# Kernel optimization log

Hardware: AMD Instinct MI355X
Metric: run time of the kernel (lower is better)

The kernel has to match this reference:

```python
import jax, jax.numpy as jnp
import numpy as np

T, B, NA = 32, 32, 5          # timesteps, envs, actions
HID, FEAT = 256, 512          # lstm hidden, cnn features
IN_DIM = FEAT + NA            # lstm input size (517)
FLAT = 64 * 7 * 7             # cnn flatten size (3136)


def _conv(x, w, b, s):
    # x: NCHW, w: OIHW, VALID padding, stride s
    y = jax.lax.conv_general_dilated(x, w, (s, s), 'VALID',
                                     dimension_numbers=('NCHW', 'OIHW', 'NCHW'))
    return y + b[None, :, None, None]


def setup_inputs() -> dict:
    key = jax.random.key(0)
    ks = jax.random.split(key, 24)
    p = lambda k, shape: (jax.random.normal(k, shape, jnp.float32) * 0.05)
    return {
        'image': jax.random.uniform(ks[0], (T * B, 3, 84, 84), jnp.float32) * 255.0,
        'last_action': jax.random.randint(ks[1], (T * B,), 0, NA),
        'done': jax.random.bernoulli(ks[2], 0.05, (T * B,)).astype(jnp.float32),
        'h0': jnp.zeros((B, HID), jnp.float32),
        'c0': jnp.zeros((B, HID), jnp.float32),
        # NatureCNN params
        'W1': p(ks[3], (32, 3, 8, 8)), 'b1': jnp.zeros((32,), jnp.float32),
        'W2': p(ks[4], (64, 32, 4, 4)), 'b2': jnp.zeros((64,), jnp.float32),
        'W3': p(ks[5], (64, 64, 3, 3)), 'b3': jnp.zeros((64,), jnp.float32),
        'Wfc': p(ks[6], (FEAT, FLAT)), 'bfc': jnp.zeros((FEAT,), jnp.float32),
        # LSTM params (torch gate order i,f,g,o)
        'W_ih': p(ks[7], (4 * HID, IN_DIM)), 'W_hh': p(ks[8], (4 * HID, HID)),
        'b_ih': jnp.zeros((4 * HID,), jnp.float32), 'b_hh': jnp.zeros((4 * HID,), jnp.float32),
        # policy MLP (hidden 64, tanh)
        'Wp1': p(ks[9], (64, HID)), 'bp1': jnp.zeros((64,), jnp.float32),
        'Wp2': p(ks[10], (NA, 64)) * 0.01, 'bp2': jnp.zeros((NA,), jnp.float32),
        # value MLP
        'Wv1': p(ks[11], (64, HID)), 'bv1': jnp.zeros((64,), jnp.float32),
        'Wv2': p(ks[12], (1, 64)), 'bv2': jnp.zeros((1,), jnp.float32),
    }


def reference(image, last_action, done, h0, c0,
              W1, b1, W2, b2, W3, b3, Wfc, bfc,
              W_ih, W_hh, b_ih, b_hh,
              Wp1, bp1, Wp2, bp2, Wv1, bv1, Wv2, bv2):
    # --- extract: NatureCNN + one-hot(last_action) ---
    x = image / 255.0
    x = jax.nn.relu(_conv(x, W1, b1, 4))   # (TB,32,20,20)
    x = jax.nn.relu(_conv(x, W2, b2, 2))   # (TB,64,9,9)
    x = jax.nn.relu(_conv(x, W3, b3, 1))   # (TB,64,7,7)
    x = x.reshape(x.shape[0], -1)
    feat = jax.nn.relu(x @ Wfc.T + bfc)    # (TB,512)
    oh = jax.nn.one_hot(last_action, NA, dtype=feat.dtype)
    xs = jnp.concatenate([feat, oh], axis=1).reshape(T, B, IN_DIM)
    ds = done.reshape(T, B)

    # --- remember: done-masked LSTM recurrence (torch gate order i,f,g,o) ---
    def step(carry, inp):
        h, c = carry
        xt, dt = inp
        m = (1.0 - dt)[:, None]
        h = h * m
        c = c * m
        g = xt @ W_ih.T + b_ih + h @ W_hh.T + b_hh   # (B, 4*HID)
        i, f, gg, o = jnp.split(g, 4, axis=1)
        c = jax.nn.sigmoid(f) * c + jax.nn.sigmoid(i) * jnp.tanh(gg)
        h = jax.nn.sigmoid(o) * jnp.tanh(c)
        return (h, c), h

    (hT, cT), hs = jax.lax.scan(step, (h0, c0), (xs, ds))
    h = hs.reshape(T * B, HID)

    # --- heads ---
    logits = jnp.tanh(h @ Wp1.T + bp1) @ Wp2.T + bp2   # (TB, NA)
    v = jnp.tanh(h @ Wv1.T + bv1) @ Wv2.T + bv2        # (TB, 1)
    return logits, v, hT, cT
```

## Files before the change

### kernel.cpp

```cpp
#include <hip/hip_runtime.h>
#include <math.h>

typedef float  f4v __attribute__((ext_vector_type(4)));
typedef short  s8v __attribute__((ext_vector_type(8)));
typedef int    i4v __attribute__((ext_vector_type(4)));

__device__ __forceinline__ float sigm(float x) { return 1.f / (1.f + expf(-x)); }
__device__ __forceinline__ unsigned short f2bf(float f) {
    unsigned int u = __float_as_uint(f);
    return (unsigned short)((u + 0x7FFF + ((u >> 16) & 1)) >> 16);
}
__device__ __forceinline__ unsigned int cvt2(float lo, float hi) {
    unsigned int r;
    asm("v_cvt_pk_bf16_f32 %0, %1, %2" : "=v"(r) : "v"(lo), "v"(hi));
    return r;
}

__global__ __launch_bounds__(256) void k_amax(const float* __restrict__ Whh,
                                              unsigned int* __restrict__ amax_bits) {
    int i = blockIdx.x * 256 + threadIdx.x;
    float v = fabsf(Whh[i]);
#pragma unroll
    for (int o = 1; o < 64; o <<= 1) v = fmaxf(v, __shfl_xor(v, o));
    if ((threadIdx.x & 63) == 0) atomicMax(amax_bits, __float_as_uint(v));
}

__global__ __launch_bounds__(256) void k_prep(const float* __restrict__ W2, const float* __restrict__ W3,
                                              const float* __restrict__ Wfc, const float* __restrict__ Wih,
                                              const float* __restrict__ W1, const float* __restrict__ Whh,
                                              const unsigned int* __restrict__ amax_bits,
                                              unsigned short* __restrict__ W2p, unsigned short* __restrict__ W3p,
                                              unsigned short* __restrict__ Wfcp, unsigned short* __restrict__ Wihp,
                                              unsigned short* __restrict__ W1p, signed char* __restrict__ Wq) {
    int i = blockIdx.x * 256 + threadIdx.x;
    if (i < 32768) {
        int co = i >> 9, k = i & 511, t = k >> 5, ci = k & 31, ky = t >> 2, kx = t & 3;
        W2p[i] = f2bf(W2[co * 512 + ci * 16 + ky * 4 + kx]);
    } else if (i < 69632) {
        int j = i - 32768;
        int co = j / 576, k = j - co * 576, t = k >> 6, ci = k & 63;
        int ky = t / 3, kx = t - ky * 3;
        W3p[j] = f2bf(W3[((co * 64 + ci) * 3 + ky) * 3 + kx]);
    } else if (i < 1675264) {
        int j = i - 69632;
        Wfcp[j] = f2bf(Wfc[j]);
    } else if (i < 2199552) {
        int j = i - 1675264;
        int n = j >> 9, k = j & 511;
        Wihp[j] = f2bf(Wih[n * 517 + k]);
    } else if (i < 2205696) {
        int j = i - 2199552;
        W1p[j] = f2bf(W1[j] * (1.f / 255.f));
    } else if (i < 2467840) {
        int j = i - 2205696;
        float amax = __uint_as_float(amax_bits[0]);
        float s = 127.f / amax;
        int qv = (int)rintf(Whh[j] * s);
        qv = qv > 127 ? 127 : (qv < -127 ? -127 : qv);
        Wq[j] = (signed char)qv;
    }
}

__global__ __launch_bounds__(512) void k_conv1(const float* __restrict__ img,
                                               const unsigned short* __restrict__ Bw,
                                               const float* __restrict__ bias,
                                               unsigned short* __restrict__ out) {
    __shared__ unsigned short sImg[21168];
    int tid = threadIdx.x;
    int lane = tid & 63, w = tid >> 6;
    int l15 = lane & 15, q = lane >> 4;
    int im = blockIdx.x;
    const float4* srcv = (const float4*)(img + im * 21168);
    unsigned int* sW = (unsigned int*)sImg;
    for (int wi = tid; wi < 5292; wi += 512) {
        float4 v = srcv[wi];
        sW[wi * 2]     = cvt2(v.x, v.y);
        sW[wi * 2 + 1] = cvt2(v.z, v.w);
    }
    __syncthreads();
    const unsigned short* Bp0 = Bw + l15 * 192 + q * 8;
    const unsigned short* Bp1 = Bw + (16 + l15) * 192 + q * 8;
    s8v bf0[6], bf1[6];
#pragma unroll
    for (int ks = 0; ks < 6; ++ks) {
        bf0[ks] = *(const s8v*)(Bp0 + ks * 32);
        bf1[ks] = *(const s8v*)(Bp1 + ks * 32);
    }
    int woff[6];
#pragma unroll
    for (int ks = 0; ks < 6; ++ks) {
        int k0 = ks * 32 + q * 8;
        int c = k0 >> 6, ky = (k0 >> 3) & 7;
        woff[ks] = c * 7056 + ky * 84;
    }
    f4v acc[4][2];
#pragma unroll
    for (int i = 0; i < 4; ++i) { acc[i][0] = (f4v){0.f,0.f,0.f,0.f}; acc[i][1] = (f4v){0.f,0.f,0.f,0.f}; }
#pragma unroll
    for (int tt = 0; tt < 4; ++tt) {
        int t = w + tt * 8;
        if (t < 25) {
            int pA = t * 16 + l15;
            int oy = pA / 20, ox = pA - oy * 20;
            const unsigned short* ab = sImg + oy * 336 + ox * 4;
#pragma unroll
            for (int ks = 0; ks < 6; ++ks) {
                s8v a = *(const s8v*)(ab + woff[ks]);
                acc[tt][0] = __builtin_amdgcn_mfma_f32_16x16x32_bf16(a, bf0[ks], acc[tt][0], 0, 0, 0);
                acc[tt][1] = __builtin_amdgcn_mfma_f32_16x16x32_bf16(a, bf1[ks], acc[tt][1], 0, 0, 0);
            }
        }
    }
    __syncthreads();
    float b0v = bias[l15], b1v = bias[16 + l15];
#pragma unroll
    for (int tt = 0; tt < 4; ++tt) {
        int t = w + tt * 8;
        if (t < 25) {
            int pc = t * 16 + q * 4;
#pragma unroll
            for (int r = 0; r < 4; r += 2) {
                float v0 = acc[tt][0][r] + b0v;     v0 = v0 > 0.f ? v0 : 0.f;
                float v1 = acc[tt][0][r + 1] + b0v; v1 = v1 > 0.f ? v1 : 0.f;
                *(unsigned int*)&sImg[l15 * 404 + pc + r] = cvt2(v0, v1);
                float u0 = acc[tt][1][r] + b1v;     u0 = u0 > 0.f ? u0 : 0.f;
                float u1 = acc[tt][1][r + 1] + b1v; u1 = u1 > 0.f ? u1 : 0.f;
                *(unsigned int*)&sImg[(16 + l15) * 404 + pc + r] = cvt2(u0, u1);
            }
        }
    }
    __syncthreads();
    const unsigned int* cw = (const unsigned int*)sImg;
    unsigned int* ow = (unsigned int*)(out + im * 12800);
    for (int i = tid; i < 6400; i += 512) {
        int n = i / 200, rem = i - n * 200;
        ow[i] = cw[n * 202 + rem];
    }
}

__global__ __launch_bounds__(256, 2) void k_conv2(const unsigned short* __restrict__ A,
                                                  const unsigned short* __restrict__ Bw,
                                                  const float* __restrict__ bias,
                                                  unsigned short* __restrict__ out) {
    __shared__ unsigned short sA[800 * 32];
    __shared__ unsigned short c2s[64][196];
    int tid = threadIdx.x;
    int lane = tid & 63, w = tid >> 6;
    int l15 = lane & 15, q = lane >> 4;
    int img0 = blockIdx.x * 2;
    char* sAb = (char*)sA;
    const s8v* srcv = (const s8v*)(A + img0 * 12800);
    for (int wi = tid; wi < 3200; wi += 256) {
        s8v v = srcv[wi];
        int f = wi * 8;
        int im = f / 12800, r = f - im * 12800, ci = r / 400, p = r - ci * 400;
#pragma unroll
        for (int j = 0; j < 8; ++j) {
            int R = im * 400 + p + j;
            int Rl = (R >> 1) + (R & 1) * 400;
            int by = (Rl * 32 + ci) * 2 ^ ((Rl & 7) << 4);
            *(unsigned short*)(sAb + by) = (unsigned short)v[j];
        }
    }
    __syncthreads();
    int Rb[3];
#pragma unroll
    for (int mf = 0; mf < 3; ++mf) {
        int t = w * 3 + mf;
        int im = t / 6;
        int pp = (t - im * 6) * 16 + l15;
        int px = pp > 80 ? 80 : pp;
        int oy = px / 9, ox = px - oy * 9;
        Rb[mf] = im * 400 + oy * 40 + ox * 2;
    }
    const unsigned short* Bp0 = Bw + l15 * 512 + q * 8;
    const unsigned short* Bp1 = Bw + (16 + l15) * 512 + q * 8;
    const unsigned short* Bp2 = Bw + (32 + l15) * 512 + q * 8;
    const unsigned short* Bp3 = Bw + (48 + l15) * 512 + q * 8;
    f4v acc[3][4];
#pragma unroll
    for (int i = 0; i < 3; ++i)
#pragma unroll
        for (int j = 0; j < 4; ++j) acc[i][j] = (f4v){0.f, 0.f, 0.f, 0.f};
#pragma unroll
    for (int s = 0; s < 16; ++s) {
        const int ky = s >> 2, kx = s & 3;
        const int d = ky * 20 + kx;
        s8v a[3];
#pragma unroll
        for (int mf = 0; mf < 3; ++mf) {
            int R = Rb[mf] + d;
            int Rl = (R >> 1) + (R & 1) * 400;
            int by = (Rl * 64 + q * 16) ^ ((Rl & 7) << 4);
            a[mf] = *(const s8v*)(sAb + by);
        }
        s8v b0 = *(const s8v*)(Bp0 + s * 32);
        s8v b1 = *(const s8v*)(Bp1 + s * 32);
        s8v b2 = *(const s8v*)(Bp2 + s * 32);
        s8v b3 = *(const s8v*)(Bp3 + s * 32);
#pragma unroll
        for (int mf = 0; mf < 3; ++mf) {
            acc[mf][0] = __builtin_amdgcn_mfma_f32_16x16x32_bf16(a[mf], b0, acc[mf][0], 0, 0, 0);
            acc[mf][1] = __builtin_amdgcn_mfma_f32_16x16x32_bf16(a[mf], b1, acc[mf][1], 0, 0, 0);
            acc[mf][2] = __builtin_amdgcn_mfma_f32_16x16x32_bf16(a[mf], b2, acc[mf][2], 0, 0, 0);
            acc[mf][3] = __builtin_amdgcn_mfma_f32_16x16x32_bf16(a[mf], b3, acc[mf][3], 0, 0, 0);
        }
    }
#pragma unroll
    for (int nf = 0; nf < 4; ++nf) {
        int co = nf * 16 + l15;
        float b = bias[co];
#pragma unroll
        for (int mf = 0; mf < 3; ++mf) {
            int rr = (w * 3 + mf) * 16 + q * 4;
#pragma unroll
            for (int r = 0; r < 4; r += 2) {
                float v0 = acc[mf][nf][r] + b;     v0 = v0 > 0.f ? v0 : 0.f;
                float v1 = acc[mf][nf][r + 1] + b; v1 = v1 > 0.f ? v1 : 0.f;
                *(unsigned int*)&c2s[co][rr + r] = cvt2(v0, v1);
            }
        }
    }
    __syncthreads();
    for (int idx = tid; idx < 10368; idx += 256) {
        int im = idx / 5184, r2 = idx - im * 5184, co = r2 / 81, p = r2 - co * 81;
        out[(img0 + im) * 5184 + r2] = c2s[co][im * 96 + p];
    }
}

__global__ __launch_bounds__(256, 2) void k_conv3(const unsigned short* __restrict__ A,
                                                  const unsigned short* __restrict__ Bw,
                                                  const float* __restrict__ bias,
                                                  unsigned short* __restrict__ out) {
    __shared__ unsigned short sA[162 * 64];
    __shared__ unsigned short c3s[64][132];
    int tid = threadIdx.x;
    int lane = tid & 63, w = tid >> 6;
    int l15 = lane & 15, q = lane >> 4;
    int img0 = blockIdx.x * 2;
    char* sAb = (char*)sA;
    const s8v* srcv = (const s8v*)(A + img0 * 5184);
    for (int wi = tid; wi < 1296; wi += 256) {
        s8v v = srcv[wi];
        int f = wi * 8;
#pragma unroll
        for (int j = 0; j < 8; ++j) {
            int fe = f + j;
            int im = fe / 5184, r = fe - im * 5184, ci = r / 81, p = r - ci * 81;
            int R = im * 81 + p;
            int by = (R * 64 + ci) * 2 ^ ((R & 7) << 4);
            *(unsigned short*)(sAb + by) = (unsigned short)v[j];
        }
    }
    __syncthreads();
    int Rb[2];
#pragma unroll
    for (int mf = 0; mf < 2; ++mf) {
        int t = w * 2 + mf;
        int im = t >> 2;
        int pp = (t & 3) * 16 + l15;
        int px = pp > 48 ? 48 : pp;
        int oy = px / 7, ox = px - oy * 7;
        Rb[mf] = im * 81 + oy * 9 + ox;
    }
    const unsigned short* Bp0 = Bw + l15 * 576 + q * 8;
    const unsigned short* Bp1 = Bw + (16 + l15) * 576 + q * 8;
    const unsigned short* Bp2 = Bw + (32 + l15) * 576 + q * 8;
    const unsigned short* Bp3 = Bw + (48 + l15) * 576 + q * 8;
    f4v acc[2][4];
#pragma unroll
    for (int i = 0; i < 2; ++i)
#pragma unroll
        for (int j = 0; j < 4; ++j) acc[i][j] = (f4v){0.f, 0.f, 0.f, 0.f};
#pragma unroll
    for (int s = 0; s < 18; ++s) {
        const int tap = s >> 1, cb2 = (s & 1) * 64;
        const int ky = tap / 3, kx = tap - ky * 3;
        const int d = ky * 9 + kx;
        s8v a0, a1;
        {
            int R = Rb[0] + d;
            int by = (R * 128 + cb2 + q * 16) ^ ((R & 7) << 4);
            a0 = *(const s8v*)(sAb + by);
        }
        {
            int R = Rb[1] + d;
            int by = (R * 128 + cb2 + q * 16) ^ ((R & 7) << 4);
            a1 = *(const s8v*)(sAb + by);
        }
        s8v b0 = *(const s8v*)(Bp0 + s * 32);
        s8v b1 = *(const s8v*)(Bp1 + s * 32);
        s8v b2 = *(const s8v*)(Bp2 + s * 32);
        s8v b3 = *(const s8v*)(Bp3 + s * 32);
        acc[0][0] = __builtin_amdgcn_mfma_f32_16x16x32_bf16(a0, b0, acc[0][0], 0, 0, 0);
        acc[0][1] = __builtin_amdgcn_mfma_f32_16x16x32_bf16(a0, b1, acc[0][1], 0, 0, 0);
        acc[0][2] = __builtin_amdgcn_mfma_f32_16x16x32_bf16(a0, b2, acc[0][2], 0, 0, 0);
        acc[0][3] = __builtin_amdgcn_mfma_f32_16x16x32_bf16(a0, b3, acc[0][3], 0, 0, 0);
        acc[1][0] = __builtin_amdgcn_mfma_f32_16x16x32_bf16(a1, b0, acc[1][0], 0, 0, 0);
        acc[1][1] = __builtin_amdgcn_mfma_f32_16x16x32_bf16(a1, b1, acc[1][1], 0, 0, 0);
        acc[1][2] = __builtin_amdgcn_mfma_f32_16x16x32_bf16(a1, b2, acc[1][2], 0, 0, 0);
        acc[1][3] = __builtin_amdgcn_mfma_f32_16x16x32_bf16(a1, b3, acc[1][3], 0, 0, 0);
    }
#pragma unroll
    for (int nf = 0; nf < 4; ++nf) {
        int co = nf * 16 + l15;
        float b = bias[co];
#pragma unroll
        for (int mf = 0; mf < 2; ++mf) {
            int rr = (w * 2 + mf) * 16 + q * 4;
#pragma unroll
            for (int r = 0; r < 4; r += 2) {
                float v0 = acc[mf][nf][r] + b;     v0 = v0 > 0.f ? v0 : 0.f;
                float v1 = acc[mf][nf][r + 1] + b; v1 = v1 > 0.f ? v1 : 0.f;
                *(unsigned int*)&c3s[co][rr + r] = cvt2(v0, v1);
            }
        }
    }
    __syncthreads();
    for (int idx = tid; idx < 6272; idx += 256) {
        int im = idx / 3136, r2 = idx - im * 3136, co = r2 / 49, p = r2 - co * 49;
        out[(img0 + im) * 3136 + r2] = c3s[co][im * 64 + p];
    }
}

__global__ __launch_bounds__(256) void k_fc(const unsigned short* __restrict__ A,
                                            const unsigned short* __restrict__ Bw,
                                            const float* __restrict__ bias,
                                            unsigned short* __restrict__ out) {
    int lane = threadIdx.x & 63, w = threadIdx.x >> 6;
    int l15 = lane & 15, q = lane >> 4;
    int m0 = blockIdx.x * 32 + (w & 1) * 16;
    int n0 = blockIdx.y * 64 + (w >> 1) * 32;
    const unsigned short* Ap = A + (m0 + l15) * 3136 + q * 8;
    const unsigned short* B0 = Bw + (n0 + l15) * 3136 + q * 8;
    const unsigned short* B1 = B0 + 16 * 3136;
    f4v acc0 = (f4v){0.f, 0.f, 0.f, 0.f}, acc1 = (f4v){0.f, 0.f, 0.f, 0.f};
    s8v av = *(const s8v*)Ap, b0 = *(const s8v*)B0, b1 = *(const s8v*)B1;
    for (int c = 0; c < 97; ++c) {
        Ap += 32; B0 += 32; B1 += 32;
        s8v nav = *(const s8v*)Ap, nb0 = *(const s8v*)B0, nb1 = *(const s8v*)B1;
        acc0 = __builtin_amdgcn_mfma_f32_16x16x32_bf16(av, b0, acc0, 0, 0, 0);
        acc1 = __builtin_amdgcn_mfma_f32_16x16x32_bf16(av, b1, acc1, 0, 0, 0);
        av = nav; b0 = nb0; b1 = nb1;
    }
    acc0 = __builtin_amdgcn_mfma_f32_16x16x32_bf16(av, b0, acc0, 0, 0, 0);
    acc1 = __builtin_amdgcn_mfma_f32_16x16x32_bf16(av, b1, acc1, 0, 0, 0);
    float bi0 = bias[n0 + l15], bi1 = bias[n0 + 16 + l15];
#pragma unroll
    for (int r = 0; r < 4; ++r) {
        int m = m0 + q * 4 + r;
        float v0 = acc0[r] + bi0; v0 = v0 > 0.f ? v0 : 0.f;
        float v1 = acc1[r] + bi1; v1 = v1 > 0.f ? v1 : 0.f;
        out[m * 512 + n0 + l15] = f2bf(v0);
        out[m * 512 + n0 + 16 + l15] = f2bf(v1);
    }
}

__global__ __launch_bounds__(256) void k_gx(const unsigned short* __restrict__ A,
                                            const unsigned short* __restrict__ Bw,
                                            const float* __restrict__ Wih,
                                            const float* __restrict__ bih,
                                            const float* __restrict__ bhh,
                                            const int* __restrict__ act,
                                            float* __restrict__ out) {
    int lane = threadIdx.x & 63, w = threadIdx.x >> 6;
    int l15 = lane & 15, q = lane >> 4;
    int m0 = blockIdx.x * 32 + (w & 1) * 16;
    int n0 = blockIdx.y * 64 + (w >> 1) * 32;
    const unsigned short* Ap = A + (m0 + l15) * 512 + q * 8;
    const unsigned short* B0 = Bw + (n0 + l15) * 512 + q * 8;
    const unsigned short* B1 = B0 + 16 * 512;
    f4v acc0 = (f4v){0.f, 0.f, 0.f, 0.f}, acc1 = (f4v){0.f, 0.f, 0.f, 0.f};
    for (int c = 0; c < 16; ++c) {
        s8v av = *(const s8v*)Ap;
        s8v b0 = *(const s8v*)B0;
        s8v b1 = *(const s8v*)B1;
        Ap += 32; B0 += 32; B1 += 32;
        acc0 = __builtin_amdgcn_mfma_f32_16x16x32_bf16(av, b0, acc0, 0, 0, 0);
        acc1 = __builtin_amdgcn_mfma_f32_16x16x32_bf16(av, b1, acc1, 0, 0, 0);
    }
    int na = n0 + l15, nb = n0 + 16 + l15;
    float ca = bih[na] + bhh[na], cb_ = bih[nb] + bhh[nb];
#pragma unroll
    for (int r = 0; r < 4; ++r) {
        int m = m0 + q * 4 + r;
        int a = act[m];
        out[m * 1024 + na] = acc0[r] + Wih[na * 517 + 512 + a] + ca;
        out[m * 1024 + nb] = acc1[r] + Wih[nb * 517 + 512 + a] + cb_;
    }
}

__global__ __launch_bounds__(1024) void k_lstm_all(const float* __restrict__ h0,
                                                   const float* __restrict__ c0,
                                                   const float* __restrict__ done,
                                                   const float* __restrict__ gx,
                                                   const signed char* __restrict__ Wq,
                                                   const unsigned int* __restrict__ amax_bits,
                                                   float* __restrict__ hs,
                                                   float* __restrict__ cb) {
    int b = blockIdx.x;
    int tid = threadIdx.x;
    int w = tid >> 6, lane = tid & 63;
    int l15 = lane & 15, q = lane >> 4;
    __shared__ float gbuf[1024];
    __shared__ float cst[256];
    __shared__ signed char hA[4][64][16];

    i4v wfr[4][4];
    const signed char* wb = Wq + (w * 64 + l15) * 256 + q * 16;
#pragma unroll
    for (int s = 0; s < 4; ++s)
#pragma unroll
        for (int kf = 0; kf < 4; ++kf)
            wfr[s][kf] = *(const i4v*)(wb + s * 16 * 256 + kf * 64);
    float sw = __uint_as_float(amax_bits[0]) * (1.f / (127.f * 127.f));

    ((int*)hA)[tid] = 0;
    __syncthreads();
    if (tid < 256) {
        int u = tid;
        cst[u] = c0[b * 256 + u];
        float m0v = 1.f - done[b];
        float hv = h0[b * 256 + u] * m0v;
        hv = hv > 1.f ? 1.f : (hv < -1.f ? -1.f : hv);
        hA[u >> 6][((u >> 4) & 3) * 16][u & 15] = (signed char)(int)rintf(hv * 127.f);
    }
    __syncthreads();

    for (int t = 0; t < 32; ++t) {
        float gxi = 0.f, gxf = 0.f, gxg = 0.f, gxo = 0.f, dcur = 0.f, dnxt = 0.f;
        if (tid < 256) {
            const float* gr = gx + (t * 32 + b) * 1024;
            gxi = gr[tid]; gxf = gr[256 + tid]; gxg = gr[512 + tid]; gxo = gr[768 + tid];
            dcur = done[t * 32 + b];
            dnxt = (t < 31) ? done[(t + 1) * 32 + b] : 1.f;
        }
        i4v acc[4];
#pragma unroll
        for (int s = 0; s < 4; ++s) acc[s] = (i4v){0, 0, 0, 0};
#pragma unroll
        for (int kf = 0; kf < 4; ++kf) {
            i4v a = *(const i4v*)&hA[kf][lane][0];
#pragma unroll
            for (int s = 0; s < 4; ++s)
                acc[s] = __builtin_amdgcn_mfma_i32_16x16x64_i8(a, wfr[s][kf], acc[s], 0, 0, 0);
        }
        if (q == 0) {
#pragma unroll
            for (int s = 0; s < 4; ++s)
                gbuf[w * 64 + s * 16 + l15] = (float)acc[s][0];
        }
        __syncthreads();
        if (tid < 256) {
            int u = tid;
            float gi = gbuf[u] * sw + gxi;
            float gf = gbuf[256 + u] * sw + gxf;
            float gg = gbuf[512 + u] * sw + gxg;
            float go = gbuf[768 + u] * sw + gxo;
            float cm = cst[u] * (1.f - dcur);
            float cn = sigm(gf) * cm + sigm(gi) * tanhf(gg);
            float hn = sigm(go) * tanhf(cn);
            cst[u] = cn;
            hs[t * 8192 + b * 256 + u] = hn;
            float hv = hn * (1.f - dnxt);
            hA[u >> 6][((u >> 4) & 3) * 16][u & 15] = (signed char)(int)rintf(hv * 127.f);
        }
        __syncthreads();
    }
    if (tid < 256) cb[b * 256 + tid] = cst[tid];
}

__global__ __launch_bounds__(256) void k_heads(const float* __restrict__ hs,
                                               const float* __restrict__ cb,
                                               const float* __restrict__ Wp1, const float* __restrict__ bp1,
                                               const float* __restrict__ Wp2, const float* __restrict__ bp2,
                                               const float* __restrict__ Wv1, const float* __restrict__ bv1,
                                               const float* __restrict__ Wv2, const float* __restrict__ bv2,
                                               float* __restrict__ out) {
    int lane = threadIdx.x & 63;
    int m = blockIdx.x * 4 + (threadIdx.x >> 6);
    const float4* hv = (const float4*)(hs + m * 256);
    const float4* wp = (const float4*)(Wp1 + lane * 256);
    const float4* wq = (const float4*)(Wv1 + lane * 256);
    float ap = 0.f, av = 0.f;
#pragma unroll 8
    for (int k = 0; k < 64; ++k) {
        float4 h4 = hv[k];
        float4 p4 = wp[k];
        float4 q4 = wq[k];
        ap += h4.x * p4.x + h4.y * p4.y + h4.z * p4.z + h4.w * p4.w;
        av += h4.x * q4.x + h4.y * q4.y + h4.z * q4.z + h4.w * q4.w;
    }
    float hp = tanhf(ap + bp1[lane]);
    float hq = tanhf(av + bv1[lane]);
#pragma unroll
    for (int j = 0; j < 5; ++j) {
        float s = hp * Wp2[j * 64 + lane];
        s += __shfl_xor(s, 1); s += __shfl_xor(s, 2); s += __shfl_xor(s, 4);
        s += __shfl_xor(s, 8); s += __shfl_xor(s, 16); s += __shfl_xor(s, 32);
        if (lane == 0) out[m * 5 + j] = s + bp2[j];
    }
    float s = hq * Wv2[lane];
    s += __shfl_xor(s, 1); s += __shfl_xor(s, 2); s += __shfl_xor(s, 4);
    s += __shfl_xor(s, 8); s += __shfl_xor(s, 16); s += __shfl_xor(s, 32);
    if (lane == 0) out[5120 + m] = s + bv2[0];

    int g = blockIdx.x * 256 + threadIdx.x;
    if (g < 8192) {
        out[6144 + g] = hs[31 * 8192 + g];
        out[6144 + 8192 + g] = cb[g];
    }
}

extern "C" void kernel_launch(void* const* d_in, const int* in_sizes, int n_in,
                              void* d_out, int out_size, void* d_ws, size_t ws_size,
                              hipStream_t stream) {
    const float* image = (const float*)d_in[0];
    const int*   act   = (const int*)d_in[1];
    const float* done  = (const float*)d_in[2];
    const float* h0    = (const float*)d_in[3];
    const float* c0    = (const float*)d_in[4];
    const float* W1    = (const float*)d_in[5];
    const float* b1    = (const float*)d_in[6];
    const float* W2    = (const float*)d_in[7];
    const float* b2    = (const float*)d_in[8];
    const float* W3    = (const float*)d_in[9];
    const float* b3    = (const float*)d_in[10];
    const float* Wfc   = (const float*)d_in[11];
    const float* bfc   = (const float*)d_in[12];
    const float* Wih   = (const float*)d_in[13];
    const float* Whh   = (const float*)d_in[14];
    const float* bih   = (const float*)d_in[15];
    const float* bhh   = (const float*)d_in[16];
    const float* Wp1   = (const float*)d_in[17];
    const float* bp1   = (const float*)d_in[18];
    const float* Wp2   = (const float*)d_in[19];
    const float* bp2   = (const float*)d_in[20];
    const float* Wv1   = (const float*)d_in[21];
    const float* bv1   = (const float*)d_in[22];
    const float* Wv2   = (const float*)d_in[23];
    const float* bv2   = (const float*)d_in[24];
    float* out = (float*)d_out;
    char* base = (char*)d_ws;

    unsigned short* a1   = (unsigned short*)(base);
    unsigned short* a2   = (unsigned short*)(base + 26214432);
    unsigned short* W2p  = (unsigned short*)(base + 36831328);
    unsigned short* W3p  = (unsigned short*)(base + 36896864);
    unsigned short* Wfcp = (unsigned short*)(base + 36970592);
    unsigned short* Wihp = (unsigned short*)(base + 40181856);
    unsigned short* W1p  = (unsigned short*)(base + 41230432);
    unsigned int*   amax = (unsigned int*)(base + 41242752);
    signed char*    Wq   = (signed char*)(base + 41242784);
    unsigned short* a3   = (unsigned short*)(base);
    unsigned short* feat = (unsigned short*)(base + 6422528);
    float* gx = (float*)(base + 7471104);
    float* hs = (float*)(base + 11665408);
    float* cb = (float*)(base + 12713984);

    hipMemsetAsync(amax, 0, 4, stream);
    k_amax<<<1024, 256, 0, stream>>>(Whh, amax);
    k_prep<<<9640, 256, 0, stream>>>(W2, W3, Wfc, Wih, W1, Whh, amax, W2p, W3p, Wfcp, Wihp, W1p, Wq);
    k_conv1<<<1024, 512, 0, stream>>>(image, W1p, b1, a1);
    k_conv2<<<512, 256, 0, stream>>>(a1, W2p, b2, a2);
    k_conv3<<<512, 256, 0, stream>>>(a2, W3p, b3, a3);
    k_fc<<<dim3(32, 8), 256, 0, stream>>>(a3, Wfcp, bfc, feat);
    k_gx<<<dim3(32, 16), 256, 0, stream>>>(feat, Wihp, Wih, bih, bhh, act, gx);
    k_lstm_all<<<32, 1024, 0, stream>>>(h0, c0, done, gx, Wq, amax, hs, cb);
    k_heads<<<256, 256, 0, stream>>>(hs, cb, Wp1, bp1, Wp2, bp2, Wv1, bv1, Wv2, bv2, out);
}
```

Baseline: 428.8 us.

## Split conv1 into half-image blocks with async global-to-LDS fp32 staging

conv1 now processes each image as two row-halves in separate 256-thread blocks, for twice as many blocks. The raw fp32 rows are copied straight into LDS with global_load_lds rather than being converted to bf16 during staging. The bf16 packing moves into the MFMA inner loop, so each A fragment reads fp32 from LDS and converts it there. The aim is to cut staging latency and register traffic and raise occupancy, at the cost of twice the LDS reads per fragment, extra conversion work, and some overlapping rows loaded by both halves.

```diff
diff --git a/kernel.cpp b/kernel.cpp
--- a/kernel.cpp
+++ b/kernel.cpp
@@ -14,6 +14,16 @@
     unsigned int r;
     asm("v_cvt_pk_bf16_f32 %0, %1, %2" : "=v"(r) : "v"(lo), "v"(hi));
     return r;
+}
+__device__ __forceinline__ s8v pack8(float4 a, float4 b) {
+    union { unsigned int u[4]; s8v v; } r;
+    r.u[0] = cvt2(a.x, a.y); r.u[1] = cvt2(a.z, a.w);
+    r.u[2] = cvt2(b.x, b.y); r.u[3] = cvt2(b.z, b.w);
+    return r.v;
+}
+__device__ __forceinline__ void gload16(const void* g, void* l) {
+    __builtin_amdgcn_global_load_lds((const __attribute__((address_space(1))) void*)g,
+                                     (__attribute__((address_space(3))) void*)l, 16, 0, 0);
 }
 
 __global__ __launch_bounds__(256) void k_amax(const float* __restrict__ Whh,
@@ -61,23 +71,36 @@
     }
 }
 
-__global__ __launch_bounds__(512) void k_conv1(const float* __restrict__ img,
-                                               const unsigned short* __restrict__ Bw,
-                                               const float* __restrict__ bias,
-                                               unsigned short* __restrict__ out) {
-    __shared__ unsigned short sImg[21168];
+__global__ __launch_bounds__(256, 3) void k_conv1(const float* __restrict__ img,
+                                                  const unsigned short* __restrict__ Bw,
+                                                  const float* __restrict__ bias,
+                                                  unsigned short* __restrict__ out) {
+    __shared__ float sF[12096];
     int tid = threadIdx.x;
     int lane = tid & 63, w = tid >> 6;
     int l15 = lane & 15, q = lane >> 4;
-    int im = blockIdx.x;
-    const float4* srcv = (const float4*)(img + im * 21168);
-    unsigned int* sW = (unsigned int*)sImg;
-    for (int wi = tid; wi < 5292; wi += 512) {
-        float4 v = srcv[wi];
-        sW[wi * 2]     = cvt2(v.x, v.y);
-        sW[wi * 2 + 1] = cvt2(v.z, v.w);
-    }
-    __syncthreads();
+    int bh = blockIdx.x & 1;
+    int im = blockIdx.x >> 1;
+    const int y0    = bh ? 40 : 0;
+    const int S     = bh ? 14784 : 16128;
+    const int fullc = bh ? 14 : 15;
+    const int tailg = bh ? 28 : 48;
+    const int t0    = bh ? 13 : 0;
+    const int nt    = bh ? 12 : 13;
+    char* sFb = (char*)sF;
+    const char* gimg = (const char*)(img + (size_t)im * 21168);
+    for (int c = 0; c < 3; ++c) {
+        const char* gb = gimg + c * 28224 + y0 * 336;
+        char* lb = sFb + c * S;
+        for (int j = w; j < fullc; j += 4) {
+            int off = j * 1024 + lane * 16;
+            gload16(gb + off, lb + off);
+        }
+        if (w == c && lane < tailg) {
+            int off = fullc * 1024 + lane * 16;
+            *(float4*)(lb + off) = *(const float4*)(gb + off);
+        }
+    }
     const unsigned short* Bp0 = Bw + l15 * 192 + q * 8;
     const unsigned short* Bp1 = Bw + (16 + l15) * 192 + q * 8;
     s8v bf0[6], bf1[6];
@@ -86,55 +109,60 @@
         bf0[ks] = *(const s8v*)(Bp0 + ks * 32);
         bf1[ks] = *(const s8v*)(Bp1 + ks * 32);
     }
-    int woff[6];
+    int koff[6];
 #pragma unroll
     for (int ks = 0; ks < 6; ++ks) {
-        int k0 = ks * 32 + q * 8;
-        int c = k0 >> 6, ky = (k0 >> 3) & 7;
-        woff[ks] = c * 7056 + ky * 84;
-    }
+        int kq = ks * 4 + q;
+        int c = kq >> 3, ky = kq & 7;
+        koff[ks] = c * S + ky * 336;
+    }
+    __syncthreads();
     f4v acc[4][2];
 #pragma unroll
     for (int i = 0; i < 4; ++i) { acc[i][0] = (f4v){0.f,0.f,0.f,0.f}; acc[i][1] = (f4v){0.f,0.f,0.f,0.f}; }
 #pragma unroll
     for (int tt = 0; tt < 4; ++tt) {
-        int t = w + tt * 8;
-        if (t < 25) {
-            int pA = t * 16 + l15;
-            int oy = pA / 20, ox = pA - oy * 20;
-            const unsigned short* ab = sImg + oy * 336 + ox * 4;
+        int li = w + tt * 4;
+        if (li < nt) {
+            int p = (t0 + li) * 16 + l15;
+            int oy = p / 20, ox = p - oy * 20;
+            int tb = (oy * 4 - y0) * 336 + ox * 16;
 #pragma unroll
             for (int ks = 0; ks < 6; ++ks) {
-                s8v a = *(const s8v*)(ab + woff[ks]);
-                acc[tt][0] = __builtin_amdgcn_mfma_f32_16x16x32_bf16(a, bf0[ks], acc[tt][0], 0, 0, 0);
-                acc[tt][1] = __builtin_amdgcn_mfma_f32_16x16x32_bf16(a, bf1[ks], acc[tt][1], 0, 0, 0);
+                float4 a0 = *(const float4*)(sFb + koff[ks] + tb);
+                float4 a1 = *(const float4*)(sFb + koff[ks] + tb + 16);
+                s8v ua = pack8(a0, a1);
+                acc[tt][0] = __builtin_amdgcn_mfma_f32_16x16x32_bf16(ua, bf0[ks], acc[tt][0], 0, 0, 0);
+                acc[tt][1] = __builtin_amdgcn_mfma_f32_16x16x32_bf16(ua, bf1[ks], acc[tt][1], 0, 0, 0);
             }
         }
     }
     __syncthreads();
+    unsigned short* cS = (unsigned short*)sFb;
     float b0v = bias[l15], b1v = bias[16 + l15];
 #pragma unroll
     for (int tt = 0; tt < 4; ++tt) {
-        int t = w + tt * 8;
-        if (t < 25) {
-            int pc = t * 16 + q * 4;
+        int li = w + tt * 4;
+        if (li < nt) {
+            int pc = li * 16 + q * 4;
 #pragma unroll
             for (int r = 0; r < 4; r += 2) {
                 float v0 = acc[tt][0][r] + b0v;     v0 = v0 > 0.f ? v0 : 0.f;
                 float v1 = acc[tt][0][r + 1] + b0v; v1 = v1 > 0.f ? v1 : 0.f;
-                *(unsigned int*)&sImg[l15 * 404 + pc + r] = cvt2(v0, v1);
+                *(unsigned int*)&cS[l15 * 212 + pc + r] = cvt2(v0, v1);
                 float u0 = acc[tt][1][r] + b1v;     u0 = u0 > 0.f ? u0 : 0.f;
                 float u1 = acc[tt][1][r + 1] + b1v; u1 = u1 > 0.f ? u1 : 0.f;
-                *(unsigned int*)&sImg[(16 + l15) * 404 + pc + r] = cvt2(u0, u1);
+                *(unsigned int*)&cS[(16 + l15) * 212 + pc + r] = cvt2(u0, u1);
             }
         }
     }
     __syncthreads();
-    const unsigned int* cw = (const unsigned int*)sImg;
-    unsigned int* ow = (unsigned int*)(out + im * 12800);
-    for (int i = tid; i < 6400; i += 512) {
-        int n = i / 200, rem = i - n * 200;
-        ow[i] = cw[n * 202 + rem];
+    int hc = nt * 8;
+    const unsigned int* cw = (const unsigned int*)cS;
+    for (int n = w; n < 32; n += 4) {
+        const unsigned int* crow = cw + n * 106;
+        unsigned int* orow = (unsigned int*)(out + (im * 32 + n) * 400 + t0 * 16);
+        for (int j = lane; j < hc; j += 64) orow[j] = crow[j];
     }
 }
 
@@ -561,7 +589,7 @@
     hipMemsetAsync(amax, 0, 4, stream);
     k_amax<<<1024, 256, 0, stream>>>(Whh, amax);
     k_prep<<<9640, 256, 0, stream>>>(W2, W3, Wfc, Wih, W1, Whh, amax, W2p, W3p, Wfcp, Wihp, W1p, Wq);
-    k_conv1<<<1024, 512, 0, stream>>>(image, W1p, b1, a1);
+    k_conv1<<<2048, 256, 0, stream>>>(image, W1p, b1, a1);
     k_conv2<<<512, 256, 0, stream>>>(a1, W2p, b2, a2);
     k_conv3<<<512, 256, 0, stream>>>(a2, W3p, b3, a3);
     k_fc<<<dim3(32, 8), 256, 0, stream>>>(a3, Wfcp, bfc, feat);
```

New measurement: 416.4 us. -2.9%, faster.
